# Performance work log

Measured on AMD Instinct MI355X. Metric: run time of the kernel, lower is better.

## Reference

```python
import jax, jax.numpy as jnp
import numpy as np

N, E, IN_FEATS, D, H, DIST_DIM, NBOUND = 10000, 160000, 128, 64, 4, 32, 31

def setup_inputs() -> dict:
    key = jax.random.key(0)
    ks = jax.random.split(key, 16)
    gain = 5.0 / 3.0  # tanh gain
    def xavier(k, shape):
        # xavier_normal over the last two dims (fan_in, fan_out) as torch does per-slice
        fan_in, fan_out = shape[-2], shape[-1]
        std = gain * np.sqrt(2.0 / (fan_in + fan_out))
        return jax.random.normal(k, shape, dtype=jnp.float32) * std
    inp = {
        'feat': jax.random.normal(ks[0], (N, IN_FEATS), dtype=jnp.float32),
        'locations': jax.random.normal(ks[1], (N, 3), dtype=jnp.float32),
        'src': jax.random.randint(ks[2], (E,), 0, N),
        'dst': jax.random.randint(ks[3], (E,), 0, N),
        'inter_ids': jax.random.randint(ks[4], (E, H), 0, N),
        'W_fc': xavier(ks[5], (IN_FEATS, H * D)),
        'embed_table': jax.random.normal(ks[6], (NBOUND + 1, DIST_DIM), dtype=jnp.float32),
        'G': xavier(ks[7], (H, DIST_DIM, D)),
        'attn_fc1': xavier(ks[8], (H, 2 * D, D)),
        'attn_fc2': xavier(ks[9], (H, 2 * D, D)),
        'attn_fc3': xavier(ks[10], (H, 2 * D, D)),
        'attn_fc': xavier(ks[11], (H, 3 * D, D)),
        'attn_out': xavier(ks[12], (H, D, 1)),
        'boundaries': jnp.linspace(0.1, 3.1, NBOUND).astype(jnp.float32),
    }
    return inp


def reference(feat, locations, W_fc, embed_table, G, attn_fc1, attn_fc2, attn_fc3,
              attn_fc, attn_out, boundaries, src, dst, inter_ids):
    n = feat.shape[0]
    h = (feat @ W_fc).reshape(n, H, D)                      # [N,H,D]
    pos = locations                                          # [N,3]
    src_pos = pos[src]                                       # [E,3]
    dst_pos = pos[dst]                                       # [E,3]
    inter_pos = pos[inter_ids]                               # [E,H,3]
    h_src = h[src]                                           # [E,H,D]
    h_dst = h[dst]                                           # [E,H,D]
    head_idx = jnp.arange(H)[None, :]
    inter_h = h[inter_ids, head_idx, :]                      # [E,H,D] per-head gather

    e_count = src.shape[0]
    dist1 = jnp.broadcast_to(jnp.linalg.norm(dst_pos - src_pos, axis=-1)[:, None], (e_count, H))
    dist2 = jnp.linalg.norm(dst_pos[:, None, :] - inter_pos, axis=-1)   # [E,H]
    dist_ = jnp.linalg.norm(src_pos[:, None, :] - inter_pos, axis=-1)   # [E,H]

    def dist_embed(dist):
        idx = jnp.searchsorted(boundaries, dist, side='left')  # torch.bucketize(right=False)
        e = embed_table[idx]                                   # [E,H,DIST_DIM]
        return jnp.einsum('ehk,hkd->ehd', e, G)                # [E,H,D]

    de1 = dist_embed(dist1)
    de2 = dist_embed(dist2)
    de_ = dist_embed(dist_)

    d1 = jnp.einsum('ehk,hkd->ehd', jnp.concatenate([h_src, de1], axis=-1), attn_fc1)
    d2 = jnp.einsum('ehk,hkd->ehd', jnp.concatenate([inter_h, de2], axis=-1), attn_fc2)
    d3 = jnp.einsum('ehk,hkd->ehd', jnp.concatenate([h_dst, de_], axis=-1), attn_fc3)

    h_c = jnp.tanh(jnp.einsum('ehk,hkd->ehd', jnp.concatenate([d1, d2, d3], axis=-1), attn_fc))
    e_score = jnp.einsum('ehd,hdo->eho', h_c, attn_out)[..., 0]        # [E,H]

    # edge softmax grouped by destination node
    m = jax.ops.segment_max(e_score, dst, num_segments=n)              # [N,H]
    ex = jnp.exp(e_score - m[dst])
    den = jax.ops.segment_sum(ex, dst, num_segments=n)                 # [N,H]
    a = ex / den[dst]                                                  # [E,H]

    ft = jax.ops.segment_sum(a[:, :, None] * h_src, dst, num_segments=n)  # [N,H,D]
    rst = jnp.mean(ft, axis=1)                                          # merge='mean' -> [N,D]
    return rst
```

## Files before the change

kernel.cpp:

```cpp
#include <hip/hip_runtime.h>
#include <hip/hip_fp16.h>
#include <math.h>

#define N_NODES 10000
#define E_EDGES 160000
#define DMODEL 64
#define H 4
#define NBOUND 31
#define SLOTS 64
#define QREC 1024

typedef _Float16 half8 __attribute__((ext_vector_type(8)));
typedef float floatx4 __attribute__((ext_vector_type(4)));

__device__ __forceinline__ void mm4(const float* __restrict__ S, int aoff,
                                    int astride, int boff, int i0, int j,
                                    int Kdim, float o[4]) {
  float a0 = 0.f, a1 = 0.f, a2 = 0.f, a3 = 0.f;
  for (int t4 = 0; t4 < (Kdim >> 2); ++t4) {
    float4 f0 = *(const float4*)&S[aoff + (i0 + 0) * astride + t4 * 4];
    float4 f1 = *(const float4*)&S[aoff + (i0 + 1) * astride + t4 * 4];
    float4 f2 = *(const float4*)&S[aoff + (i0 + 2) * astride + t4 * 4];
    float4 f3 = *(const float4*)&S[aoff + (i0 + 3) * astride + t4 * 4];
    float b0 = S[boff + (t4 * 4 + 0) * 64 + j];
    float b1 = S[boff + (t4 * 4 + 1) * 64 + j];
    float b2 = S[boff + (t4 * 4 + 2) * 64 + j];
    float b3 = S[boff + (t4 * 4 + 3) * 64 + j];
    a0 += f0.x * b0 + f0.y * b1 + f0.z * b2 + f0.w * b3;
    a1 += f1.x * b0 + f1.y * b1 + f1.z * b2 + f1.w * b3;
    a2 += f2.x * b0 + f2.y * b1 + f2.z * b2 + f2.w * b3;
    a3 += f3.x * b0 + f3.y * b1 + f3.z * b2 + f3.w * b3;
  }
  o[0] = a0; o[1] = a1; o[2] = a2; o[3] = a3;
}

__device__ __forceinline__ int didx(const float* __restrict__ bnd2, float d) {
  int g = (int)(d * 10.0f);
  g = (g < 0) ? 0 : ((g > 31) ? 31 : g);
  g += (bnd2[g + 1] < d) ? 1 : 0;
  g -= (bnd2[g] >= d) ? 1 : 0;
  return g;
}

__global__ __launch_bounds__(512) void prep_kernel(
    const float* __restrict__ fc1, const float* __restrict__ fc2,
    const float* __restrict__ fc3, const float* __restrict__ fcc,
    const float* __restrict__ Wfc, const float* __restrict__ G,
    const float* __restrict__ emb, const float* __restrict__ pos,
    __half* __restrict__ bigWT, __half* __restrict__ U16,
    int* __restrict__ cnt, float4* __restrict__ pos4) {
  __shared__ __align__(16) float S[12288];
  int bi = blockIdx.x;
  int tid = threadIdx.x;
  if (bi >= 24) {
    int n = (bi - 24) * 512 + tid;
    if (n < N_NODES) {
      cnt[n] = 0;
      pos4[n] = make_float4(pos[n * 3], pos[n * 3 + 1], pos[n * 3 + 2], 0.f);
    }
    return;
  }
  int chain = (bi >= 12);
  int kh = chain ? (bi - 12) : bi;
  int k = kh >> 2, h = kh & 3;
  const float* fck = (k == 0) ? fc1 : (k == 1) ? fc2 : fc3;
  fck += h * 128 * 64;
  const float* F = fcc + h * 192 * 64 + k * 64 * 64;
  int j = tid & 63, ig = tid >> 6;
  float o[4];
  if (!chain) {
    #pragma unroll
    for (int u = 0; u < 2; ++u) {
      ((float4*)S)[u * 512 + tid] = ((const float4*)F)[u * 512 + tid];
      ((float4*)(S + 4096))[u * 512 + tid] = ((const float4*)fck)[u * 512 + tid];
    }
    __syncthreads();
    #pragma unroll
    for (int rg = 0; rg < 2; ++rg) {
      int i0 = ig * 8 + rg * 4;
      mm4(S, 4096, 64, 0, i0, j, 64, o);
      S[8192 + (i0 + 0) * 64 + j] = o[0];
      S[8192 + (i0 + 1) * 64 + j] = o[1];
      S[8192 + (i0 + 2) * 64 + j] = o[2];
      S[8192 + (i0 + 3) * 64 + j] = o[3];
    }
    __syncthreads();
    #pragma unroll
    for (int u = 0; u < 2; ++u) {
      int fi = u * 512 + tid;
      int i = fi >> 4, c4 = fi & 15;
      ((float4*)(S + 4096))[fi] = ((const float4*)(Wfc + i * 256 + h * 64))[c4];
    }
    __syncthreads();
    if (k == 0) {
      #pragma unroll
      for (int u = 0; u < 8; ++u) {
        int idx = u * 512 + tid;
        int i = idx >> 6, jj = idx & 63;
        bigWT[(h * 64 + jj) * 128 + i] = __float2half(S[4096 + idx]);
      }
    }
    #pragma unroll
    for (int rg = 0; rg < 2; ++rg) {
      int i0 = ig * 8 + rg * 4;
      mm4(S, 4096, 64, 8192, i0, j, 64, o);
      int rb = ((k + 1) * 256 + h * 64 + j) * 128;
      bigWT[rb + i0 + 0] = __float2half(o[0]);
      bigWT[rb + i0 + 1] = __float2half(o[1]);
      bigWT[rb + i0 + 2] = __float2half(o[2]);
      bigWT[rb + i0 + 3] = __float2half(o[3]);
    }
    __syncthreads();
    #pragma unroll
    for (int u = 0; u < 2; ++u) {
      int fi = u * 512 + tid;
      int i = fi >> 4, c4 = fi & 15;
      ((float4*)(S + 4096))[fi] =
          ((const float4*)(Wfc + (64 + i) * 256 + h * 64))[c4];
    }
    __syncthreads();
    if (k == 0) {
      #pragma unroll
      for (int u = 0; u < 8; ++u) {
        int idx = u * 512 + tid;
        int i = idx >> 6, jj = idx & 63;
        bigWT[(h * 64 + jj) * 128 + 64 + i] = __float2half(S[4096 + idx]);
      }
    }
    #pragma unroll
    for (int rg = 0; rg < 2; ++rg) {
      int i0 = ig * 8 + rg * 4;
      mm4(S, 4096, 64, 8192, i0, j, 64, o);
      int rb = ((k + 1) * 256 + h * 64 + j) * 128;
      bigWT[rb + 64 + i0 + 0] = __float2half(o[0]);
      bigWT[rb + 64 + i0 + 1] = __float2half(o[1]);
      bigWT[rb + 64 + i0 + 2] = __float2half(o[2]);
      bigWT[rb + 64 + i0 + 3] = __float2half(o[3]);
    }
    return;
  }
  #pragma unroll
  for (int u = 0; u < 2; ++u) {
    ((float4*)S)[u * 512 + tid] = ((const float4*)F)[u * 512 + tid];
    ((float4*)(S + 4096))[u * 512 + tid] =
        ((const float4*)(fck + 4096))[u * 512 + tid];
  }
  __syncthreads();
  #pragma unroll
  for (int rg = 0; rg < 2; ++rg) {
    int i0 = ig * 8 + rg * 4;
    mm4(S, 4096, 64, 0, i0, j, 64, o);
    S[8192 + (i0 + 0) * 64 + j] = o[0];
    S[8192 + (i0 + 1) * 64 + j] = o[1];
    S[8192 + (i0 + 2) * 64 + j] = o[2];
    S[8192 + (i0 + 3) * 64 + j] = o[3];
  }
  __syncthreads();
  ((float4*)S)[tid] = ((const float4*)(G + h * 2048))[tid];
  if (tid < 256) ((float4*)(S + 2048))[tid] = ((const float4*)emb)[tid];
  __syncthreads();
  {
    int i0 = ig * 4;
    mm4(S, 0, 64, 8192, i0, j, 64, o);
    S[3072 + (i0 + 0) * 64 + j] = o[0];
    S[3072 + (i0 + 1) * 64 + j] = o[1];
    S[3072 + (i0 + 2) * 64 + j] = o[2];
    S[3072 + (i0 + 3) * 64 + j] = o[3];
  }
  __syncthreads();
  {
    int i0 = ig * 4;
    mm4(S, 2048, 32, 3072, i0, j, 32, o);
    int base = k * 8192 + h * 2048;
    U16[base + (i0 + 0) * 64 + j] = __float2half(o[0]);
    U16[base + (i0 + 1) * 64 + j] = __float2half(o[1]);
    U16[base + (i0 + 2) * 64 + j] = __float2half(o[2]);
    U16[base + (i0 + 3) * 64 + j] = __float2half(o[3]);
  }
}

#define EROW 264

__global__ __launch_bounds__(256) void gemm_edge_kernel(
    const float* __restrict__ feat, const __half* __restrict__ bigWT,
    __half* __restrict__ qall, const float4* __restrict__ pos4,
    const int* __restrict__ src, const int* __restrict__ dst,
    const int* __restrict__ inter, const float* __restrict__ boundaries,
    int* __restrict__ cnt, uint4* __restrict__ ebuf) {
  __shared__ __align__(16) __half Esm[4][16][EROW];
  __shared__ float Sb[48];
  int bi = blockIdx.x;
  int tid = threadIdx.x;
  if (bi >= 628) {
    if (tid < NBOUND) Sb[tid + 1] = boundaries[tid];
    if (tid == NBOUND) { Sb[0] = -INFINITY; Sb[32] = INFINITY; }
    __syncthreads();
    int e = (bi - 628) * 256 + tid;
    int s = src[e], t = dst[e];
    int4 iv = *(const int4*)&inter[e * 4];
    int itarr[4] = {iv.x, iv.y, iv.z, iv.w};
    float4 sp = pos4[s];
    float4 tp = pos4[t];
    float dx = tp.x - sp.x, dy = tp.y - sp.y, dz = tp.z - sp.z;
    float dist1 = sqrtf(dx * dx + dy * dy + dz * dz);
    unsigned i1 = (unsigned)didx(Sb, dist1);
    unsigned w3 = 0, q20 = 0, q_0 = 0;
    #pragma unroll
    for (int hh = 0; hh < 4; ++hh) {
      float4 ip = pos4[itarr[hh]];
      float ax = tp.x - ip.x, ay = tp.y - ip.y, az = tp.z - ip.z;
      float dist2 = sqrtf(ax * ax + ay * ay + az * az);
      float bx = sp.x - ip.x, by = sp.y - ip.y, bz = sp.z - ip.z;
      float dist_ = sqrtf(bx * bx + by * by + bz * bz);
      unsigned idx2 = (unsigned)didx(Sb, dist2);
      unsigned idx_ = (unsigned)didx(Sb, dist_);
      if (hh == 0) { q20 = idx2; q_0 = idx_; }
      else w3 |= (idx2 | (idx_ << 5)) << ((hh - 1) * 10);
    }
    uint4 rec;
    rec.x = (unsigned)s | ((unsigned)itarr[0] << 16);
    rec.y = (unsigned)itarr[1] | ((unsigned)itarr[2] << 16);
    rec.z = (unsigned)itarr[3] | (i1 << 16) | (q20 << 21) | (q_0 << 26);
    rec.w = w3;
    int p = atomicAdd(&cnt[t], 1);
    if (p < SLOTS) ebuf[t * SLOTS + p] = rec;
    return;
  }
  int bx = bi % 157, by = bi / 157;
  int wv = tid >> 6, l = tid & 63;
  int m0 = bx * 64 + wv * 16;
  int n0 = by * 256;
  int lm = l & 15, lk = (l >> 4) * 8;
  int arow = m0 + lm;
  if (arow >= N_NODES) arow = N_NODES - 1;
  const float* fp = feat + arow * 128 + lk;
  const _Float16* bp = (const _Float16*)bigWT + lk;
  half8 a[4];
  #pragma unroll
  for (int kt = 0; kt < 4; ++kt) {
    float4 u0 = *(const float4*)(fp + kt * 32);
    float4 u1 = *(const float4*)(fp + kt * 32 + 4);
    half8 t;
    t[0] = (_Float16)u0.x; t[1] = (_Float16)u0.y;
    t[2] = (_Float16)u0.z; t[3] = (_Float16)u0.w;
    t[4] = (_Float16)u1.x; t[5] = (_Float16)u1.y;
    t[6] = (_Float16)u1.z; t[7] = (_Float16)u1.w;
    a[kt] = t;
  }
  #pragma unroll
  for (int nt = 0; nt < 16; ++nt) {
    floatx4 acc = (floatx4){0.f, 0.f, 0.f, 0.f};
    #pragma unroll
    for (int kt = 0; kt < 4; ++kt) {
      half8 b = *(const half8*)(bp + (n0 + nt * 16 + lm) * 128 + kt * 32);
      acc = __builtin_amdgcn_mfma_f32_16x16x32_f16(a[kt], b, acc, 0, 0, 0);
    }
    int dd = nt * 16 + lm;
    #pragma unroll
    for (int r4 = 0; r4 < 4; ++r4)
      Esm[wv][(l >> 4) * 4 + r4][dd] = __float2half(acc[r4]);
  }
  __syncthreads();
  int row = l >> 2;
  int j0 = (l & 3) * 64;
  int m = m0 + row;
  if (m < N_NODES) {
    #pragma unroll
    for (int u = 0; u < 8; ++u) {
      uint4 v = *(const uint4*)&Esm[wv][row][j0 + u * 8];
      *(uint4*)&qall[m * QREC + by * 256 + j0 + u * 8] = v;
    }
  }
}

__device__ __forceinline__ float dpp_bfly_sum16(float v) {
  int x;
  x = __builtin_amdgcn_update_dpp(0, __float_as_int(v), 0xB1, 0xf, 0xf, true);
  v += __int_as_float(x);
  x = __builtin_amdgcn_update_dpp(0, __float_as_int(v), 0x4E, 0xf, 0xf, true);
  v += __int_as_float(x);
  x = __builtin_amdgcn_update_dpp(0, __float_as_int(v), 0x141, 0xf, 0xf, true);
  v += __int_as_float(x);
  x = __builtin_amdgcn_update_dpp(0, __float_as_int(v), 0x140, 0xf, 0xf, true);
  v += __int_as_float(x);
  return v;
}

union H4u { uint2 u; __half2 h[2]; };

__device__ __forceinline__ float tanh_dot(H4u A, H4u B, H4u C, H4u X, H4u Y,
                                          H4u Z, float4 a4) {
  __half2 z0 = __hadd2(__hadd2(A.h[0], B.h[0]), __hadd2(C.h[0], X.h[0]));
  z0 = __hadd2(z0, __hadd2(Y.h[0], Z.h[0]));
  __half2 z1 = __hadd2(__hadd2(A.h[1], B.h[1]), __hadd2(C.h[1], X.h[1]));
  z1 = __hadd2(z1, __hadd2(Y.h[1], Z.h[1]));
  float2 f0 = __half22float2(z0);
  float2 f1 = __half22float2(z1);
  const float K = 2.885390082f;
  float p0 = __builtin_amdgcn_exp2f(f0.x * K);
  float p1 = __builtin_amdgcn_exp2f(f0.y * K);
  float p2 = __builtin_amdgcn_exp2f(f1.x * K);
  float p3 = __builtin_amdgcn_exp2f(f1.y * K);
  float r0 = __builtin_amdgcn_rcpf(p0 + 1.0f);
  float r1 = __builtin_amdgcn_rcpf(p1 + 1.0f);
  float r2 = __builtin_amdgcn_rcpf(p2 + 1.0f);
  float r3 = __builtin_amdgcn_rcpf(p3 + 1.0f);
  float dot = a4.x * r0;
  dot = fmaf(a4.y, r1, dot);
  dot = fmaf(a4.z, r2, dot);
  dot = fmaf(a4.w, r3, dot);
  float asum = (a4.x + a4.y) + (a4.z + a4.w);
  return fmaf(-2.0f, dot, asum);
}

__device__ __forceinline__ float4 h4_to_f4(uint2 u) {
  union { uint2 ui; __half2 h[2]; } cc;
  cc.ui = u;
  float2 a = __half22float2(cc.h[0]);
  float2 b = __half22float2(cc.h[1]);
  return make_float4(a.x, a.y, b.x, b.y);
}

__device__ __forceinline__ void dec_rec(uint4 r, int h, int* s, int* it,
                                        unsigned* i1, unsigned* q2,
                                        unsigned* q_) {
  *s = (int)(r.x & 0xffff);
  *it = (h == 0) ? (int)(r.x >> 16)
      : (h == 1) ? (int)(r.y & 0xffff)
      : (h == 2) ? (int)(r.y >> 16) : (int)(r.z & 0xffff);
  *i1 = (r.z >> 16) & 31;
  if (h == 0) {
    *q2 = (r.z >> 21) & 31;
    *q_ = (r.z >> 26) & 31;
  } else {
    unsigned f = r.w >> ((h - 1) * 10);
    *q2 = f & 31;
    *q_ = (f >> 5) & 31;
  }
}

__global__ __launch_bounds__(256) void score_agg_kernel(
    const int* __restrict__ cnt, const uint4* __restrict__ ebuf,
    const __half* __restrict__ qall, const __half* __restrict__ U16,
    const float* __restrict__ aout, float* __restrict__ out) {
  __shared__ uint4 recs[SLOTS];
  __shared__ float4 sm_num[4][64];
  __shared__ float sm_den[4][4];
  int tid = threadIdx.x;
  int w = tid >> 6, lane = tid & 63;
  int h = lane >> 4, c = lane & 15;
  int n = blockIdx.x;
  int deg = cnt[n];
  if (deg > SLOTS) deg = SLOTS;
  if (tid < deg) recs[tid] = ebuf[n * SLOTS + tid];
  H4u C;
  C.u = *(const uint2*)(qall + n * QREC + 768 + h * 64 + c * 4);
  const float4 a4 = *((const float4*)(aout + h * 64) + c);
  __syncthreads();
  float4 num = make_float4(0.f, 0.f, 0.f, 0.f);
  float den = 0.f;
  int hc4 = h * 64 + c * 4;
  for (int i = w; i < deg; i += 8) {
    int iB = i + 4;
    int vB = (iB < deg);
    uint4 rA = recs[i];
    uint4 rB = recs[vB ? iB : i];
    int sA, itA, sB, itB;
    unsigned i1A, q2A, q_A, i1B, q2B, q_B;
    dec_rec(rA, h, &sA, &itA, &i1A, &q2A, &q_A);
    dec_rec(rB, h, &sB, &itB, &i1B, &q2B, &q_B);
    H4u A0, B0, X0, Y0, Z0, A1, B1, X1, Y1, Z1;
    uint2 hr0, hr1;
    hr0 = *(const uint2*)(qall + sA * QREC + hc4);
    A0.u = *(const uint2*)(qall + sA * QREC + 256 + hc4);
    B0.u = *(const uint2*)(qall + itA * QREC + 512 + hc4);
    X0.u = *(const uint2*)(U16 + (h * 32 + (int)i1A) * 64 + c * 4);
    Y0.u = *(const uint2*)(U16 + 8192 + (h * 32 + (int)q2A) * 64 + c * 4);
    Z0.u = *(const uint2*)(U16 + 16384 + (h * 32 + (int)q_A) * 64 + c * 4);
    hr1 = *(const uint2*)(qall + sB * QREC + hc4);
    A1.u = *(const uint2*)(qall + sB * QREC + 256 + hc4);
    B1.u = *(const uint2*)(qall + itB * QREC + 512 + hc4);
    X1.u = *(const uint2*)(U16 + (h * 32 + (int)i1B) * 64 + c * 4);
    Y1.u = *(const uint2*)(U16 + 8192 + (h * 32 + (int)q2B) * 64 + c * 4);
    Z1.u = *(const uint2*)(U16 + 16384 + (h * 32 + (int)q_B) * 64 + c * 4);
    float v0 = tanh_dot(A0, B0, C, X0, Y0, Z0, a4);
    float v1 = tanh_dot(A1, B1, C, X1, Y1, Z1, a4);
    v0 = dpp_bfly_sum16(v0);
    v1 = dpp_bfly_sum16(v1);
    float ex0 = __expf(v0);
    float ex1 = vB ? __expf(v1) : 0.f;
    float4 hv0 = h4_to_f4(hr0);
    float4 hv1 = h4_to_f4(hr1);
    num.x += ex0 * hv0.x + ex1 * hv1.x;
    num.y += ex0 * hv0.y + ex1 * hv1.y;
    num.z += ex0 * hv0.z + ex1 * hv1.z;
    num.w += ex0 * hv0.w + ex1 * hv1.w;
    den += ex0 + ex1;
  }
  sm_num[w][lane] = num;
  if (c == 0) sm_den[w][h] = den;
  __syncthreads();
  if (tid < 64) {
    float4 n0 = sm_num[0][lane], n1 = sm_num[1][lane];
    float4 n2 = sm_num[2][lane], n3 = sm_num[3][lane];
    float dt = sm_den[0][h] + sm_den[1][h] + sm_den[2][h] + sm_den[3][h];
    float4 t = make_float4(0.f, 0.f, 0.f, 0.f);
    if (deg > 0) {
      float inv = 1.0f / dt;
      t.x = (n0.x + n1.x + n2.x + n3.x) * inv;
      t.y = (n0.y + n1.y + n2.y + n3.y) * inv;
      t.z = (n0.z + n1.z + n2.z + n3.z) * inv;
      t.w = (n0.w + n1.w + n2.w + n3.w) * inv;
    }
    t.x += __shfl_xor(t.x, 16); t.y += __shfl_xor(t.y, 16);
    t.z += __shfl_xor(t.z, 16); t.w += __shfl_xor(t.w, 16);
    t.x += __shfl_xor(t.x, 32); t.y += __shfl_xor(t.y, 32);
    t.z += __shfl_xor(t.z, 32); t.w += __shfl_xor(t.w, 32);
    if (h == 0) {
      t.x *= 0.25f; t.y *= 0.25f; t.z *= 0.25f; t.w *= 0.25f;
      *(float4*)&out[n * 64 + c * 4] = t;
    }
  }
}

extern "C" void kernel_launch(void* const* d_in, const int* in_sizes, int n_in,
                              void* d_out, int out_size, void* d_ws,
                              size_t ws_size, hipStream_t stream) {
  const float* feat = (const float*)d_in[0];
  const float* loc = (const float*)d_in[1];
  const int* src = (const int*)d_in[2];
  const int* dst = (const int*)d_in[3];
  const int* inter = (const int*)d_in[4];
  const float* Wfc = (const float*)d_in[5];
  const float* emb = (const float*)d_in[6];
  const float* G = (const float*)d_in[7];
  const float* fc1 = (const float*)d_in[8];
  const float* fc2 = (const float*)d_in[9];
  const float* fc3 = (const float*)d_in[10];
  const float* fcc = (const float*)d_in[11];
  const float* aout = (const float*)d_in[12];
  const float* bnd = (const float*)d_in[13];
  float* out = (float*)d_out;

  __half* qall = (__half*)d_ws;
  __half* bigWT = qall + N_NODES * QREC;
  __half* U16 = bigWT + 1024 * 128;
  uint4* ebuf = (uint4*)(U16 + 3 * H * 2048);
  int* cnt = (int*)(ebuf + N_NODES * SLOTS);
  float4* pos4 = (float4*)(cnt + N_NODES);

  prep_kernel<<<44, 512, 0, stream>>>(fc1, fc2, fc3, fcc, Wfc, G, emb, loc,
                                      bigWT, U16, cnt, pos4);
  gemm_edge_kernel<<<1253, 256, 0, stream>>>(feat, bigWT, qall, pos4, src, dst,
                                             inter, bnd, cnt, ebuf);
  score_agg_kernel<<<N_NODES, 256, 0, stream>>>(cnt, ebuf, qall, U16, aout,
                                                out);
}
```

Baseline: 178.8 us.

## Split prep weight-folding across more blocks and shrink edge/GEMM blocks

The prep kernel now gives each 64-row half of the W_fc folding its own block (36 compute blocks instead of 24), which removes the serial second pass. The fused GEMM/edge kernel drops from 256-thread to 128-thread blocks, with half-height GEMM tiles and twice as many edge blocks. Edge blocks are also scheduled first so their atomics and scattered writes overlap with GEMM work. The aim is more parallelism and better load balance, at the cost of more blocks, more redundant shared-memory setup, and less reuse of the B operand per block.

Result: no change. 178.4 us (-0.2%).

```diff
diff --git a/kernel.cpp b/kernel.cpp
--- a/kernel.cpp
+++ b/kernel.cpp
@@ -52,23 +52,23 @@
   __shared__ __align__(16) float S[12288];
   int bi = blockIdx.x;
   int tid = threadIdx.x;
-  if (bi >= 24) {
-    int n = (bi - 24) * 512 + tid;
+  if (bi >= 36) {
+    int n = (bi - 36) * 512 + tid;
     if (n < N_NODES) {
       cnt[n] = 0;
       pos4[n] = make_float4(pos[n * 3], pos[n * 3 + 1], pos[n * 3 + 2], 0.f);
     }
     return;
   }
-  int chain = (bi >= 12);
-  int kh = chain ? (bi - 12) : bi;
+  int ca = bi / 12;
+  int kh = bi % 12;
   int k = kh >> 2, h = kh & 3;
   const float* fck = (k == 0) ? fc1 : (k == 1) ? fc2 : fc3;
   fck += h * 128 * 64;
   const float* F = fcc + h * 192 * 64 + k * 64 * 64;
   int j = tid & 63, ig = tid >> 6;
   float o[4];
-  if (!chain) {
+  if (ca < 2) {
     #pragma unroll
     for (int u = 0; u < 2; ++u) {
       ((float4*)S)[u * 512 + tid] = ((const float4*)F)[u * 512 + tid];
@@ -85,11 +85,13 @@
       S[8192 + (i0 + 3) * 64 + j] = o[3];
     }
     __syncthreads();
+    int rbase = (ca == 0) ? 0 : 64;
     #pragma unroll
     for (int u = 0; u < 2; ++u) {
       int fi = u * 512 + tid;
       int i = fi >> 4, c4 = fi & 15;
-      ((float4*)(S + 4096))[fi] = ((const float4*)(Wfc + i * 256 + h * 64))[c4];
+      ((float4*)(S + 4096))[fi] =
+          ((const float4*)(Wfc + (rbase + i) * 256 + h * 64))[c4];
     }
     __syncthreads();
     if (k == 0) {
@@ -97,45 +99,18 @@
       for (int u = 0; u < 8; ++u) {
         int idx = u * 512 + tid;
         int i = idx >> 6, jj = idx & 63;
-        bigWT[(h * 64 + jj) * 128 + i] = __float2half(S[4096 + idx]);
+        bigWT[(h * 64 + jj) * 128 + rbase + i] = __float2half(S[4096 + idx]);
       }
     }
     #pragma unroll
     for (int rg = 0; rg < 2; ++rg) {
       int i0 = ig * 8 + rg * 4;
       mm4(S, 4096, 64, 8192, i0, j, 64, o);
-      int rb = ((k + 1) * 256 + h * 64 + j) * 128;
+      int rb = ((k + 1) * 256 + h * 64 + j) * 128 + rbase;
       bigWT[rb + i0 + 0] = __float2half(o[0]);
       bigWT[rb + i0 + 1] = __float2half(o[1]);
       bigWT[rb + i0 + 2] = __float2half(o[2]);
       bigWT[rb + i0 + 3] = __float2half(o[3]);
-    }
-    __syncthreads();
-    #pragma unroll
-    for (int u = 0; u < 2; ++u) {
-      int fi = u * 512 + tid;
-      int i = fi >> 4, c4 = fi & 15;
-      ((float4*)(S + 4096))[fi] =
-          ((const float4*)(Wfc + (64 + i) * 256 + h * 64))[c4];
-    }
-    __syncthreads();
-    if (k == 0) {
-      #pragma unroll
-      for (int u = 0; u < 8; ++u) {
-        int idx = u * 512 + tid;
-        int i = idx >> 6, jj = idx & 63;
-        bigWT[(h * 64 + jj) * 128 + 64 + i] = __float2half(S[4096 + idx]);
-      }
-    }
-    #pragma unroll
-    for (int rg = 0; rg < 2; ++rg) {
-      int i0 = ig * 8 + rg * 4;
-      mm4(S, 4096, 64, 8192, i0, j, 64, o);
-      int rb = ((k + 1) * 256 + h * 64 + j) * 128;
-      bigWT[rb + 64 + i0 + 0] = __float2half(o[0]);
-      bigWT[rb + 64 + i0 + 1] = __float2half(o[1]);
-      bigWT[rb + 64 + i0 + 2] = __float2half(o[2]);
-      bigWT[rb + 64 + i0 + 3] = __float2half(o[3]);
     }
     return;
   }
@@ -180,22 +155,23 @@
 }
 
 #define EROW 264
-
-__global__ __launch_bounds__(256) void gemm_edge_kernel(
+#define NEDGE_BLK 1250
+
+__global__ __launch_bounds__(128) void gemm_edge_kernel(
     const float* __restrict__ feat, const __half* __restrict__ bigWT,
     __half* __restrict__ qall, const float4* __restrict__ pos4,
     const int* __restrict__ src, const int* __restrict__ dst,
     const int* __restrict__ inter, const float* __restrict__ boundaries,
     int* __restrict__ cnt, uint4* __restrict__ ebuf) {
-  __shared__ __align__(16) __half Esm[4][16][EROW];
+  __shared__ __align__(16) __half Esm[2][16][EROW];
   __shared__ float Sb[48];
   int bi = blockIdx.x;
   int tid = threadIdx.x;
-  if (bi >= 628) {
+  if (bi < NEDGE_BLK) {
     if (tid < NBOUND) Sb[tid + 1] = boundaries[tid];
     if (tid == NBOUND) { Sb[0] = -INFINITY; Sb[32] = INFINITY; }
     __syncthreads();
-    int e = (bi - 628) * 256 + tid;
+    int e = bi * 128 + tid;
     int s = src[e], t = dst[e];
     int4 iv = *(const int4*)&inter[e * 4];
     int itarr[4] = {iv.x, iv.y, iv.z, iv.w};
@@ -226,9 +202,10 @@
     if (p < SLOTS) ebuf[t * SLOTS + p] = rec;
     return;
   }
-  int bx = bi % 157, by = bi / 157;
+  int gi = bi - NEDGE_BLK;
+  int bx = gi % 313, by = gi / 313;
   int wv = tid >> 6, l = tid & 63;
-  int m0 = bx * 64 + wv * 16;
+  int m0 = bx * 32 + wv * 16;
   int n0 = by * 256;
   int lm = l & 15, lk = (l >> 4) * 8;
   int arow = m0 + lm;
@@ -449,9 +426,9 @@
   int* cnt = (int*)(ebuf + N_NODES * SLOTS);
   float4* pos4 = (float4*)(cnt + N_NODES);
 
-  prep_kernel<<<44, 512, 0, stream>>>(fc1, fc2, fc3, fcc, Wfc, G, emb, loc,
+  prep_kernel<<<56, 512, 0, stream>>>(fc1, fc2, fc3, fcc, Wfc, G, emb, loc,
                                       bigWT, U16, cnt, pos4);
-  gemm_edge_kernel<<<1253, 256, 0, stream>>>(feat, bigWT, qall, pos4, src, dst,
+  gemm_edge_kernel<<<2502, 128, 0, stream>>>(feat, bigWT, qall, pos4, src, dst,
                                              inter, bnd, cnt, ebuf);
   score_agg_kernel<<<N_NODES, 256, 0, stream>>>(cnt, ebuf, qall, U16, aout,
                                                 out);
```
